# Performance work log

Measured on AMD Instinct MI355X. Metric: run time of the kernel, lower is better.

## Reference

```python
import jax, jax.numpy as jnp
import numpy as np

L, H, NH, F = 6, 1024, 16, 4096
B, S = 4, 512
D = H // NH
LN_EPS = 1e-12
GELU_C = 0.7978845608028654  # sqrt(2/pi)


def gelu_new(x):
    return 0.5 * x * (1.0 + jnp.tanh(GELU_C * (x + 0.044715 * x * x * x)))


def layer_norm(x, ln):
    # ln: [2, H] -> gamma, beta
    m = jnp.mean(x, axis=-1, keepdims=True)
    v = jnp.mean(jnp.square(x - m), axis=-1, keepdims=True)
    return (x - m) * jax.lax.rsqrt(v + LN_EPS) * ln[0] + ln[1]


def attention(q_in, kv_in, mask, qkv_w, qkv_b):
    # qkv_w: [3, H, H], qkv_b: [3, H]; mask: [B, S_kv] (1 = keep)
    b, s_q, _ = q_in.shape
    s_kv = kv_in.shape[1]
    q = (q_in @ qkv_w[0] + qkv_b[0]).reshape(b, s_q, NH, D)
    k = (kv_in @ qkv_w[1] + qkv_b[1]).reshape(b, s_kv, NH, D)
    v = (kv_in @ qkv_w[2] + qkv_b[2]).reshape(b, s_kv, NH, D)
    scale = 1.0 / (D ** 0.5)
    score = jnp.einsum('bind,bjnd->bnij', q, k) * scale  # [B, NH, Sq, Skv]
    adder = (1.0 - mask.astype(score.dtype))[:, None, None, :] * -10000.0
    prob = jax.nn.softmax(score + adder, axis=-1)
    out = jnp.einsum('bnij,bjnd->bind', prob, v)
    return out.reshape(b, s_q, H)


def _forward(hidden_states, encoder_hidden_states, attention_mask, encoder_attention_mask,
             sa_qkv_w, sa_qkv_b, sa_out_w, sa_out_b, sa_ln,
             ca_qkv_w, ca_qkv_b, ca_out_w, ca_out_b, ca_ln,
             o1_w, o1_b, o1_ln, ffn_w, ffn_b, o2_w, o2_b, o2_ln):
    h = hidden_states
    for i in range(L):
        # self attention + dense/dropout/LN (residual = h)
        self_vec = attention(h, h, attention_mask, sa_qkv_w[i], sa_qkv_b[i])
        attn_out = layer_norm(self_vec @ sa_out_w[i] + sa_out_b[i] + h, sa_ln[i])
        # cross attention + dense/dropout/LN (residual = h, per original code)
        cross_vec = attention(h, encoder_hidden_states, encoder_attention_mask,
                              ca_qkv_w[i], ca_qkv_b[i])
        cross_out = layer_norm(cross_vec @ ca_out_w[i] + ca_out_b[i] + h, ca_ln[i])
        # output_1: dense(attn_out) + cross_out, then LN
        attn_out = layer_norm(attn_out @ o1_w[i] + o1_b[i] + cross_out, o1_ln[i])
        # FFN with gelu_new, output_2: dense(inter) + attn_out, then LN
        inter = gelu_new(attn_out @ ffn_w[i] + ffn_b[i])
        h = layer_norm(inter @ o2_w[i] + o2_b[i] + attn_out, o2_ln[i])
    return h


def setup_inputs() -> dict:
    key = jax.random.key(0)
    ks = jax.random.split(key, 16)
    std = 0.02
    w = lambda k, shape: (jax.random.normal(k, shape, jnp.float32) * std)
    ln_init = jnp.stack([jnp.ones((L, H), jnp.float32), jnp.zeros((L, H), jnp.float32)], axis=1)
    return {
        'hidden_states': jax.random.normal(ks[0], (B, S, H), jnp.float32),
        'encoder_hidden_states': jax.random.normal(ks[1], (B, S, H), jnp.float32),
        'attention_mask': jnp.ones((B, S), jnp.int32),
        'encoder_attention_mask': jnp.ones((B, S), jnp.int32),
        'sa_qkv_w': w(ks[2], (L, 3, H, H)), 'sa_qkv_b': w(ks[3], (L, 3, H)),
        'sa_out_w': w(ks[4], (L, H, H)), 'sa_out_b': w(ks[5], (L, H)), 'sa_ln': ln_init,
        'ca_qkv_w': w(ks[6], (L, 3, H, H)), 'ca_qkv_b': w(ks[7], (L, 3, H)),
        'ca_out_w': w(ks[8], (L, H, H)), 'ca_out_b': w(ks[9], (L, H)), 'ca_ln': ln_init,
        'o1_w': w(ks[10], (L, H, H)), 'o1_b': w(ks[11], (L, H)), 'o1_ln': ln_init,
        'ffn_w': w(ks[12], (L, H, F)), 'ffn_b': w(ks[13], (L, F)),
        'o2_w': w(ks[14], (L, F, H)), 'o2_b': w(ks[15], (L, H)), 'o2_ln': ln_init,
    }


def reference(hidden_states, encoder_hidden_states, attention_mask, encoder_attention_mask,
              sa_qkv_w, sa_qkv_b, sa_out_w, sa_out_b, sa_ln,
              ca_qkv_w, ca_qkv_b, ca_out_w, ca_out_b, ca_ln,
              o1_w, o1_b, o1_ln, ffn_w, ffn_b, o2_w, o2_b, o2_ln):
    return _forward(hidden_states, encoder_hidden_states, attention_mask, encoder_attention_mask,
                    sa_qkv_w, sa_qkv_b, sa_out_w, sa_out_b, sa_ln,
                    ca_qkv_w, ca_qkv_b, ca_out_w, ca_out_b, ca_ln,
                    o1_w, o1_b, o1_ln, ffn_w, ffn_b, o2_w, o2_b, o2_ln)
```

## Files before the change

kernel.cpp:

```cpp
#include <hip/hip_runtime.h>


#define LNUM 6
#define HDIM 1024
#define NHEAD 16
#define DHEAD 64
#define BDIM 4
#define SDIM 512
#define FDIM 4096
#define MROWS (BDIM * SDIM)
#define HSQ (HDIM * HDIM)

typedef __bf16 bf16_t;
typedef bf16_t bf16x8 __attribute__((ext_vector_type(8)));
typedef float f32x4 __attribute__((ext_vector_type(4)));

__device__ __forceinline__ float bf2f(unsigned short u) {
    union { unsigned int i; float f; } x;
    x.i = ((unsigned int)u) << 16;
    return x.f;
}

__device__ __forceinline__ unsigned short f2bf(float f) {
    union { float f; unsigned int i; } u;
    u.f = f;
    unsigned int x = u.i;
    unsigned int lsb = (x >> 16) & 1u;
    x += 0x7fffu + lsb;
    return (unsigned short)(x >> 16);
}

__device__ __forceinline__ void async16(const unsigned short* g, unsigned short* l) {
    __builtin_amdgcn_global_load_lds(
        (const __attribute__((address_space(1))) unsigned int*)g,
        (__attribute__((address_space(3))) unsigned int*)l, 16, 0, 0);
}

template<int N>
__device__ __forceinline__ void s_wait_vmcnt() {
    asm volatile("s_waitcnt vmcnt(%0)" :: "n"(N) : "memory");
}

template<int BM, int BN, bool GELU, bool OUTBF16>
__global__ __launch_bounds__(256) void mfma_gemm(
    const unsigned short* __restrict__ A,
    const unsigned short* __restrict__ BT,
    const float* __restrict__ bias,
    void* __restrict__ Cv,
    int M, int N, int K)
{
    constexpr int BK = 64;
    constexpr int MI = BM / 32;
    constexpr int NJ = BN / 32;
    constexpr int LPT = BM / 32 + BN / 32;

    __shared__ unsigned short As[2][BM][BK];
    __shared__ unsigned short Bs[2][BN][BK];

    const int t = threadIdx.x;
    const int w = t >> 6;
    const int lane = t & 63;
    const int quad = lane >> 4;
    const int cm = lane & 15;
    const int wrow = (w >> 1) * (BM / 2);
    const int wcol = (w & 1) * (BN / 2);
    const int row0 = blockIdx.x * BM;
    const int col0 = blockIdx.y * BN;

    f32x4 acc[MI][NJ] = {};

    const int lrow = lane >> 3;
    const int lcol = ((lane & 7) ^ lrow) * 8;
    const int sw = cm & 7;

    auto stage = [&](int buf, int k0) {
#pragma unroll
        for (int j = 0; j < BM / 32; ++j) {
            int mb = w * (BM / 4) + j * 8;
            async16(A + (size_t)(row0 + mb + lrow) * K + k0 + lcol, &As[buf][mb][0]);
        }
#pragma unroll
        for (int j = 0; j < BN / 32; ++j) {
            int nb = w * (BN / 4) + j * 8;
            async16(BT + (size_t)(col0 + nb + lrow) * K + k0 + lcol, &Bs[buf][nb][0]);
        }
    };

    const int NT = K / BK;
    stage(0, 0);
    int cur = 0;
    for (int ti = 0; ti < NT; ++ti) {
        if (ti + 1 < NT) {
            stage(cur ^ 1, (ti + 1) * BK);
            s_wait_vmcnt<LPT>();
        } else {
            s_wait_vmcnt<0>();
        }
        __builtin_amdgcn_s_barrier();
        __builtin_amdgcn_sched_barrier(0);

#pragma unroll
        for (int kk = 0; kk < BK; kk += 32) {
            const int cc = kk >> 3;
            bf16x8 av[MI], bv[NJ];
#pragma unroll
            for (int i = 0; i < MI; ++i)
                av[i] = *(const bf16x8*)&As[cur][wrow + 16 * i + cm][((cc + quad) ^ sw) * 8];
#pragma unroll
            for (int j = 0; j < NJ; ++j)
                bv[j] = *(const bf16x8*)&Bs[cur][wcol + 16 * j + cm][((cc + quad) ^ sw) * 8];
#pragma unroll
            for (int i = 0; i < MI; ++i)
#pragma unroll
                for (int j = 0; j < NJ; ++j)
                    acc[i][j] = __builtin_amdgcn_mfma_f32_16x16x32_bf16(
                        av[i], bv[j], acc[i][j], 0, 0, 0);
        }

        __builtin_amdgcn_sched_barrier(0);
        __builtin_amdgcn_s_barrier();
        cur ^= 1;
    }

#pragma unroll
    for (int j = 0; j < NJ; ++j) {
        int col = col0 + wcol + 16 * j + cm;
        float bb = bias[col];
#pragma unroll
        for (int i = 0; i < MI; ++i) {
#pragma unroll
            for (int r = 0; r < 4; ++r) {
                int row = row0 + wrow + 16 * i + quad * 4 + r;
                float c = acc[i][j][r] + bb;
                if (GELU) {
                    float u = 0.7978845608028654f * (c + 0.044715f * c * c * c);
                    c = 0.5f * c * (1.0f + tanhf(u));
                }
                if (OUTBF16)
                    ((unsigned short*)Cv)[(size_t)row * N + col] = f2bf(c);
                else
                    ((float*)Cv)[(size_t)row * N + col] = c;
            }
        }
    }
}

template<int BM>
__global__ __launch_bounds__(256) void mfma_gemm_qkv(
    const unsigned short* __restrict__ Aq,
    const unsigned short* __restrict__ Akv,
    const unsigned short* __restrict__ BT,
    const float* __restrict__ bias,
    unsigned short* __restrict__ qo,
    unsigned short* __restrict__ ko,
    unsigned short* __restrict__ vo,
    int M, int K)
{
    constexpr int BK = 64;
    constexpr int BN = 64;
    constexpr int MI = BM / 32;
    constexpr int NJ = 2;
    constexpr int LPT = BM / 32 + BN / 32;

    __shared__ unsigned short As[2][BM][BK];
    __shared__ unsigned short Bs[2][BN][BK];

    const int t = threadIdx.x;
    const int w = t >> 6;
    const int lane = t & 63;
    const int quad = lane >> 4;
    const int cm = lane & 15;
    const int wrow = (w >> 1) * (BM / 2);
    const int wcol = (w & 1) * 32;
    const int row0 = blockIdx.x * BM;
    const int col0 = blockIdx.y * BN;

    const int which = col0 >> 10;
    const unsigned short* __restrict__ A = (which == 0) ? Aq : Akv;

    f32x4 acc[MI][NJ] = {};

    const int lrow = lane >> 3;
    const int lcol = ((lane & 7) ^ lrow) * 8;
    const int sw = cm & 7;

    auto stage = [&](int buf, int k0) {
#pragma unroll
        for (int j = 0; j < BM / 32; ++j) {
            int mb = w * (BM / 4) + j * 8;
            async16(A + (size_t)(row0 + mb + lrow) * K + k0 + lcol, &As[buf][mb][0]);
        }
#pragma unroll
        for (int j = 0; j < NJ; ++j) {
            int nb = w * 16 + j * 8;
            async16(BT + (size_t)(col0 + nb + lrow) * K + k0 + lcol, &Bs[buf][nb][0]);
        }
    };

    const int NT = K / BK;
    stage(0, 0);
    int cur = 0;
    for (int ti = 0; ti < NT; ++ti) {
        if (ti + 1 < NT) {
            stage(cur ^ 1, (ti + 1) * BK);
            s_wait_vmcnt<LPT>();
        } else {
            s_wait_vmcnt<0>();
        }
        __builtin_amdgcn_s_barrier();
        __builtin_amdgcn_sched_barrier(0);

#pragma unroll
        for (int kk = 0; kk < BK; kk += 32) {
            const int cc = kk >> 3;
            bf16x8 av[MI], bv[NJ];
#pragma unroll
            for (int i = 0; i < MI; ++i)
                av[i] = *(const bf16x8*)&As[cur][wrow + 16 * i + cm][((cc + quad) ^ sw) * 8];
#pragma unroll
            for (int j = 0; j < NJ; ++j)
                bv[j] = *(const bf16x8*)&Bs[cur][wcol + 16 * j + cm][((cc + quad) ^ sw) * 8];
#pragma unroll
            for (int i = 0; i < MI; ++i)
#pragma unroll
                for (int j = 0; j < NJ; ++j)
                    acc[i][j] = __builtin_amdgcn_mfma_f32_16x16x32_bf16(
                        av[i], bv[j], acc[i][j], 0, 0, 0);
        }

        __builtin_amdgcn_sched_barrier(0);
        __builtin_amdgcn_s_barrier();
        cur ^= 1;
    }

    unsigned short* dst = (which == 0) ? qo : (which == 1) ? ko : vo;
    const int cbase = col0 & 1023;

#pragma unroll
    for (int j = 0; j < NJ; ++j) {
        int col = col0 + wcol + 16 * j + cm;
        float bb = bias[col];
        int coll = cbase + wcol + 16 * j + cm;
#pragma unroll
        for (int i = 0; i < MI; ++i) {
#pragma unroll
            for (int r = 0; r < 4; ++r) {
                int row = row0 + wrow + 16 * i + quad * 4 + r;
                dst[(size_t)row * HDIM + coll] = f2bf(acc[i][j][r] + bb);
            }
        }
    }
}

__global__ __launch_bounds__(256) void flash_attn(
    const unsigned short* __restrict__ q,
    const unsigned short* __restrict__ k,
    const unsigned short* __restrict__ v,
    const int* __restrict__ mask,
    unsigned short* __restrict__ ctx)
{
    __shared__ unsigned short Qs[64][64];
    __shared__ unsigned short Ks[64][64];
    __shared__ unsigned short Vs[64][72];
    __shared__ unsigned short Ps[4][16][72];

    const int t = threadIdx.x;
    const int w = t >> 6;
    const int lane = t & 63;
    const int quad = lane >> 4;
    const int cm = lane & 15;
    const int sw = cm & 7;

    const int q0 = blockIdx.x * 64;
    const int h = blockIdx.y;
    const int b = blockIdx.z;
    const size_t rowbase = (size_t)b * SDIM;
    const int hoff = h * DHEAD;

#pragma unroll
    for (int l = 0; l < 2; ++l) {
        int idx = t + l * 256;
        int r = idx >> 3;
        int c = idx & 7;
        *(uint4*)&Qs[r][((c ^ (r & 7)) * 8)] =
            *(const uint4*)(q + (rowbase + q0 + r) * HDIM + hoff + c * 8);
    }

    float m_prev[4] = {-1e30f, -1e30f, -1e30f, -1e30f};
    float l_sum[4] = {0.0f, 0.0f, 0.0f, 0.0f};
    f32x4 oacc[4] = {};

    for (int j0 = 0; j0 < SDIM; j0 += 64) {
        __syncthreads();
#pragma unroll
        for (int l = 0; l < 2; ++l) {
            int idx = t + l * 256;
            int r = idx >> 3;
            int c = idx & 7;
            *(uint4*)&Ks[r][((c ^ (r & 7)) * 8)] =
                *(const uint4*)(k + (rowbase + j0 + r) * HDIM + hoff + c * 8);
        }
#pragma unroll
        for (int l = 0; l < 4; ++l) {
            int idx = t + l * 256;
            int jj = idx >> 4;
            int d0 = (idx & 15) * 4;
            ushort4 vv = *(const ushort4*)(v + (rowbase + j0 + jj) * HDIM + hoff + d0);
            Vs[d0 + 0][jj] = vv.x;
            Vs[d0 + 1][jj] = vv.y;
            Vs[d0 + 2][jj] = vv.z;
            Vs[d0 + 3][jj] = vv.w;
        }
        __syncthreads();

        f32x4 sacc[4] = {};
#pragma unroll
        for (int kk = 0; kk < 64; kk += 32) {
            const int cc = kk >> 3;
            bf16x8 av = *(const bf16x8*)&Qs[w * 16 + cm][((cc + quad) ^ sw) * 8];
#pragma unroll
            for (int j2 = 0; j2 < 4; ++j2) {
                bf16x8 bv = *(const bf16x8*)&Ks[j2 * 16 + cm][((cc + quad) ^ sw) * 8];
                sacc[j2] = __builtin_amdgcn_mfma_f32_16x16x32_bf16(av, bv, sacc[j2], 0, 0, 0);
            }
        }

        float madd[4];
#pragma unroll
        for (int j2 = 0; j2 < 4; ++j2)
            madd[j2] = (1.0f - (float)mask[b * SDIM + j0 + j2 * 16 + cm]) * -10000.0f;

#pragma unroll
        for (int r = 0; r < 4; ++r) {
            float s0 = sacc[0][r] * 0.125f + madd[0];
            float s1 = sacc[1][r] * 0.125f + madd[1];
            float s2 = sacc[2][r] * 0.125f + madd[2];
            float s3 = sacc[3][r] * 0.125f + madd[3];
            float rm = fmaxf(fmaxf(s0, s1), fmaxf(s2, s3));
#pragma unroll
            for (int mo = 1; mo < 16; mo <<= 1)
                rm = fmaxf(rm, __shfl_xor(rm, mo, 64));
            float new_m = fmaxf(m_prev[r], rm);
            float alpha = __expf(m_prev[r] - new_m);
            m_prev[r] = new_m;
            float p0 = __expf(s0 - new_m);
            float p1 = __expf(s1 - new_m);
            float p2 = __expf(s2 - new_m);
            float p3 = __expf(s3 - new_m);
            float rs = p0 + p1 + p2 + p3;
#pragma unroll
            for (int mo = 1; mo < 16; mo <<= 1)
                rs += __shfl_xor(rs, mo, 64);
            l_sum[r] = l_sum[r] * alpha + rs;
#pragma unroll
            for (int d2 = 0; d2 < 4; ++d2)
                oacc[d2][r] *= alpha;
            int prow = quad * 4 + r;
            Ps[w][prow][0 * 16 + cm] = f2bf(p0);
            Ps[w][prow][1 * 16 + cm] = f2bf(p1);
            Ps[w][prow][2 * 16 + cm] = f2bf(p2);
            Ps[w][prow][3 * 16 + cm] = f2bf(p3);
        }

#pragma unroll
        for (int kk = 0; kk < 64; kk += 32) {
            bf16x8 pa = *(const bf16x8*)&Ps[w][cm][kk + quad * 8];
#pragma unroll
            for (int d2 = 0; d2 < 4; ++d2) {
                bf16x8 bv = *(const bf16x8*)&Vs[d2 * 16 + cm][kk + quad * 8];
                oacc[d2] = __builtin_amdgcn_mfma_f32_16x16x32_bf16(pa, bv, oacc[d2], 0, 0, 0);
            }
        }
    }

#pragma unroll
    for (int r = 0; r < 4; ++r) {
        float inv = 1.0f / l_sum[r];
        int row = q0 + w * 16 + quad * 4 + r;
#pragma unroll
        for (int d2 = 0; d2 < 4; ++d2) {
            ctx[(rowbase + row) * HDIM + hoff + d2 * 16 + cm] = f2bf(oacc[d2][r] * inv);
        }
    }
}

__global__ __launch_bounds__(256) void convtrans_all(
    const float* __restrict__ sqkv, const float* __restrict__ sout,
    const float* __restrict__ cqkv, const float* __restrict__ cout,
    const float* __restrict__ o1w,  const float* __restrict__ ffnw,
    const float* __restrict__ o2w,
    unsigned short* __restrict__ dq,  unsigned short* __restrict__ dso,
    unsigned short* __restrict__ dcq, unsigned short* __restrict__ dco,
    unsigned short* __restrict__ do1, unsigned short* __restrict__ dffn,
    unsigned short* __restrict__ do2)
{
    __shared__ unsigned short tile[64][72];
    const int bid = blockIdx.x;
    const float* src;
    unsigned short* dst;
    int K, N, tt;
    if (bid < 2304) {
        int m = bid >> 8;
        tt = bid & 255;
        K = HDIM; N = HDIM;
        if (m < 3)      { src = sqkv + (size_t)m * HSQ;       dst = dq  + (size_t)m * HSQ; }
        else if (m < 6) { src = cqkv + (size_t)(m - 3) * HSQ; dst = dcq + (size_t)(m - 3) * HSQ; }
        else if (m == 6){ src = sout; dst = dso; }
        else if (m == 7){ src = cout; dst = dco; }
        else            { src = o1w;  dst = do1; }
    } else if (bid < 3328) {
        tt = bid - 2304; K = HDIM; N = FDIM; src = ffnw; dst = dffn;
    } else {
        tt = bid - 3328; K = FDIM; N = HDIM; src = o2w; dst = do2;
    }
    const int tn = N >> 6;
    const int n0 = (tt % tn) * 64;
    const int k0 = (tt / tn) * 64;
    const int t = threadIdx.x;
#pragma unroll
    for (int l = 0; l < 4; ++l) {
        int idx = t + l * 256;
        int kk = idx >> 4;
        int nn = (idx & 15) * 4;
        float4 v = *(const float4*)(src + (size_t)(k0 + kk) * N + n0 + nn);
        tile[nn + 0][kk] = f2bf(v.x);
        tile[nn + 1][kk] = f2bf(v.y);
        tile[nn + 2][kk] = f2bf(v.z);
        tile[nn + 3][kk] = f2bf(v.w);
    }
    __syncthreads();
#pragma unroll
    for (int l = 0; l < 2; ++l) {
        int c = t + l * 256;
        int nn = c >> 3;
        int kk = (c & 7) * 8;
        *(uint4*)(dst + (size_t)(n0 + nn) * K + k0 + kk) = *(const uint4*)&tile[nn][kk];
    }
}

template<bool OUTF32>
__global__ __launch_bounds__(256) void ln_kernel(
    const float* __restrict__ x, const unsigned short* __restrict__ resid,
    const float* __restrict__ ln, void* __restrict__ out)
{
    const int row = blockIdx.x;
    const float* xr = x + (size_t)row * HDIM;
    const unsigned short* rr = resid + (size_t)row * HDIM;
    const int t = threadIdx.x;
    __shared__ float red[4];

    float4 xv = ((const float4*)xr)[t];
    ushort4 rv = ((const ushort4*)rr)[t];
    float z[4];
    z[0] = xv.x + bf2f(rv.x);
    z[1] = xv.y + bf2f(rv.y);
    z[2] = xv.z + bf2f(rv.z);
    z[3] = xv.w + bf2f(rv.w);
    float s = z[0] + z[1] + z[2] + z[3];
#pragma unroll
    for (int off = 32; off > 0; off >>= 1) s += __shfl_down(s, off, 64);
    if ((t & 63) == 0) red[t >> 6] = s;
    __syncthreads();
    s = red[0] + red[1] + red[2] + red[3];
    float mean = s * (1.0f / (float)HDIM);

    float vs = 0.0f;
#pragma unroll
    for (int i = 0; i < 4; ++i) {
        float d = z[i] - mean;
        vs += d * d;
    }
#pragma unroll
    for (int off = 32; off > 0; off >>= 1) vs += __shfl_down(vs, off, 64);
    __syncthreads();
    if ((t & 63) == 0) red[t >> 6] = vs;
    __syncthreads();
    vs = red[0] + red[1] + red[2] + red[3];
    float inv = rsqrtf(vs * (1.0f / (float)HDIM) + 1e-12f);

    const float* g = ln + 4 * t;
    const float* bb = ln + HDIM + 4 * t;
    if (OUTF32) {
        float4 o;
        o.x = (z[0] - mean) * inv * g[0] + bb[0];
        o.y = (z[1] - mean) * inv * g[1] + bb[1];
        o.z = (z[2] - mean) * inv * g[2] + bb[2];
        o.w = (z[3] - mean) * inv * g[3] + bb[3];
        ((float4*)((float*)out + (size_t)row * HDIM))[t] = o;
    } else {
        ushort4 o;
        o.x = f2bf((z[0] - mean) * inv * g[0] + bb[0]);
        o.y = f2bf((z[1] - mean) * inv * g[1] + bb[1]);
        o.z = f2bf((z[2] - mean) * inv * g[2] + bb[2]);
        o.w = f2bf((z[3] - mean) * inv * g[3] + bb[3]);
        ((ushort4*)((unsigned short*)out + (size_t)row * HDIM))[t] = o;
    }
}

__global__ __launch_bounds__(256) void cvt_bf16_kernel(
    const float* __restrict__ in, unsigned short* __restrict__ out, int n4)
{
    int i = blockIdx.x * 256 + threadIdx.x;
    if (i < n4) {
        float4 v = ((const float4*)in)[i];
        ushort4 o;
        o.x = f2bf(v.x); o.y = f2bf(v.y); o.z = f2bf(v.z); o.w = f2bf(v.w);
        ((ushort4*)out)[i] = o;
    }
}

extern "C" void kernel_launch(void* const* d_in, const int* in_sizes, int n_in,
                              void* d_out, int out_size, void* d_ws, size_t ws_size,
                              hipStream_t stream)
{
    const float* in_hidden = (const float*)d_in[0];
    const float* enc_f     = (const float*)d_in[1];
    const int* attn_mask   = (const int*)d_in[2];
    const int* enc_attn_mask = (const int*)d_in[3];
    const float* sa_qkv_w  = (const float*)d_in[4];
    const float* sa_qkv_b  = (const float*)d_in[5];
    const float* sa_out_w  = (const float*)d_in[6];
    const float* sa_out_b  = (const float*)d_in[7];
    const float* sa_ln     = (const float*)d_in[8];
    const float* ca_qkv_w  = (const float*)d_in[9];
    const float* ca_qkv_b  = (const float*)d_in[10];
    const float* ca_out_w  = (const float*)d_in[11];
    const float* ca_out_b  = (const float*)d_in[12];
    const float* ca_ln     = (const float*)d_in[13];
    const float* o1_w      = (const float*)d_in[14];
    const float* o1_b      = (const float*)d_in[15];
    const float* o1_ln     = (const float*)d_in[16];
    const float* ffn_w     = (const float*)d_in[17];
    const float* ffn_b     = (const float*)d_in[18];
    const float* o2_w      = (const float*)d_in[19];
    const float* o2_b      = (const float*)d_in[20];
    const float* o2_ln     = (const float*)d_in[21];

    const size_t MH  = (size_t)MROWS * HDIM;
    const size_t Hsq = (size_t)HDIM * HDIM;
    const size_t HF  = (size_t)HDIM * FDIM;

    char* p = (char*)d_ws;
    unsigned short* wbf = (unsigned short*)p; p += (9 * Hsq + 2 * HF) * 2;
    float* t2     = (float*)p; p += MH * 4;
    unsigned short* qb     = (unsigned short*)p; p += MH * 2;
    unsigned short* kb     = (unsigned short*)p; p += MH * 2;
    unsigned short* vb     = (unsigned short*)p; p += MH * 2;
    unsigned short* ctx    = (unsigned short*)p; p += MH * 2;
    unsigned short* h      = (unsigned short*)p; p += MH * 2;
    unsigned short* enc_bf = (unsigned short*)p; p += MH * 2;
    unsigned short* attn1  = (unsigned short*)p; p += MH * 2;
    unsigned short* crossb = (unsigned short*)p; p += MH * 2;
    unsigned short* attn2  = (unsigned short*)p; p += MH * 2;
    unsigned short* tmp8b  = (unsigned short*)p; p += (size_t)MROWS * FDIM * 2;

    unsigned short* w_saqkv = wbf;
    unsigned short* w_saout = wbf + 3 * Hsq;
    unsigned short* w_caqkv = wbf + 4 * Hsq;
    unsigned short* w_caout = wbf + 7 * Hsq;
    unsigned short* w_o1    = wbf + 8 * Hsq;
    unsigned short* w_ffn   = wbf + 9 * Hsq;
    unsigned short* w_o2    = wbf + 9 * Hsq + HF;

    cvt_bf16_kernel<<<(MH / 4 + 255) / 256, 256, 0, stream>>>(in_hidden, h, MH / 4);
    cvt_bf16_kernel<<<(MH / 4 + 255) / 256, 256, 0, stream>>>(enc_f, enc_bf, MH / 4);

    for (int l = 0; l < LNUM; ++l) {
        convtrans_all<<<4352, 256, 0, stream>>>(
            sa_qkv_w + (size_t)l * 3 * Hsq, sa_out_w + (size_t)l * Hsq,
            ca_qkv_w + (size_t)l * 3 * Hsq, ca_out_w + (size_t)l * Hsq,
            o1_w + (size_t)l * Hsq, ffn_w + (size_t)l * HF, o2_w + (size_t)l * HF,
            w_saqkv, w_saout, w_caqkv, w_caout, w_o1, w_ffn, w_o2);

        mfma_gemm_qkv<64><<<dim3(MROWS / 64, 3072 / 64), 256, 0, stream>>>(
            h, h, w_saqkv, sa_qkv_b + (size_t)l * 3 * HDIM, qb, kb, vb, MROWS, HDIM);
        flash_attn<<<dim3(SDIM / 64, NHEAD, BDIM), 256, 0, stream>>>(
            qb, kb, vb, attn_mask, ctx);
        mfma_gemm<64, 64, false, false><<<dim3(MROWS / 64, HDIM / 64), 256, 0, stream>>>(
            ctx, w_saout, sa_out_b + (size_t)l * HDIM, t2, MROWS, HDIM, HDIM);
        ln_kernel<false><<<MROWS, 256, 0, stream>>>(t2, h, sa_ln + (size_t)l * 2 * HDIM, attn1);

        mfma_gemm_qkv<64><<<dim3(MROWS / 64, 3072 / 64), 256, 0, stream>>>(
            h, enc_bf, w_caqkv, ca_qkv_b + (size_t)l * 3 * HDIM, qb, kb, vb, MROWS, HDIM);
        flash_attn<<<dim3(SDIM / 64, NHEAD, BDIM), 256, 0, stream>>>(
            qb, kb, vb, enc_attn_mask, ctx);
        mfma_gemm<64, 64, false, false><<<dim3(MROWS / 64, HDIM / 64), 256, 0, stream>>>(
            ctx, w_caout, ca_out_b + (size_t)l * HDIM, t2, MROWS, HDIM, HDIM);
        ln_kernel<false><<<MROWS, 256, 0, stream>>>(t2, h, ca_ln + (size_t)l * 2 * HDIM, crossb);

        mfma_gemm<64, 64, false, false><<<dim3(MROWS / 64, HDIM / 64), 256, 0, stream>>>(
            attn1, w_o1, o1_b + (size_t)l * HDIM, t2, MROWS, HDIM, HDIM);
        ln_kernel<false><<<MROWS, 256, 0, stream>>>(t2, crossb, o1_ln + (size_t)l * 2 * HDIM, attn2);

        mfma_gemm<64, 128, true, true><<<dim3(MROWS / 64, FDIM / 128), 256, 0, stream>>>(
            attn2, w_ffn, ffn_b + (size_t)l * FDIM, tmp8b, MROWS, FDIM, HDIM);
        mfma_gemm<64, 64, false, false><<<dim3(MROWS / 64, HDIM / 64), 256, 0, stream>>>(
            tmp8b, w_o2, o2_b + (size_t)l * HDIM, t2, MROWS, HDIM, FDIM);
        if (l == LNUM - 1)
            ln_kernel<true><<<MROWS, 256, 0, stream>>>(
                t2, attn2, o2_ln + (size_t)l * 2 * HDIM, (float*)d_out);
        else
            ln_kernel<false><<<MROWS, 256, 0, stream>>>(
                t2, attn2, o2_ln + (size_t)l * 2 * HDIM, h);
    }
}
```

Before: 2.012 ms.

## Batch self and cross attention branches into shared launches; triple-buffer GEMM loads

```diff
diff --git a/kernel.cpp b/kernel.cpp
--- a/kernel.cpp
+++ b/kernel.cpp
@@ -52,10 +52,10 @@
     constexpr int BK = 64;
     constexpr int MI = BM / 32;
     constexpr int NJ = BN / 32;
-    constexpr int LPT = BM / 32 + BN / 32;
-
-    __shared__ unsigned short As[2][BM][BK];
-    __shared__ unsigned short Bs[2][BN][BK];
+    constexpr int LPT = MI + NJ;
+
+    __shared__ unsigned short As[3][BM][BK];
+    __shared__ unsigned short Bs[3][BN][BK];
 
     const int t = threadIdx.x;
     const int w = t >> 6;
@@ -71,7 +71,7 @@
 
     const int lrow = lane >> 3;
     const int lcol = ((lane & 7) ^ lrow) * 8;
-    const int sw = cm & 7;
+    const int sw = cm & 15 & 7;
 
     auto stage = [&](int buf, int k0) {
 #pragma unroll
@@ -88,10 +88,13 @@
 
     const int NT = K / BK;
     stage(0, 0);
-    int cur = 0;
+    stage(1, BK);
+    int c0 = 0, c1 = 1, c2 = 2;
     for (int ti = 0; ti < NT; ++ti) {
-        if (ti + 1 < NT) {
-            stage(cur ^ 1, (ti + 1) * BK);
+        if (ti + 2 < NT) {
+            stage(c2, (ti + 2) * BK);
+            s_wait_vmcnt<2 * LPT>();
+        } else if (ti + 1 < NT) {
             s_wait_vmcnt<LPT>();
         } else {
             s_wait_vmcnt<0>();
@@ -105,10 +108,10 @@
             bf16x8 av[MI], bv[NJ];
 #pragma unroll
             for (int i = 0; i < MI; ++i)
-                av[i] = *(const bf16x8*)&As[cur][wrow + 16 * i + cm][((cc + quad) ^ sw) * 8];
+                av[i] = *(const bf16x8*)&As[c0][wrow + 16 * i + cm][((cc + quad) ^ sw) * 8];
 #pragma unroll
             for (int j = 0; j < NJ; ++j)
-                bv[j] = *(const bf16x8*)&Bs[cur][wcol + 16 * j + cm][((cc + quad) ^ sw) * 8];
+                bv[j] = *(const bf16x8*)&Bs[c0][wcol + 16 * j + cm][((cc + quad) ^ sw) * 8];
 #pragma unroll
             for (int i = 0; i < MI; ++i)
 #pragma unroll
@@ -119,7 +122,7 @@
 
         __builtin_amdgcn_sched_barrier(0);
         __builtin_amdgcn_s_barrier();
-        cur ^= 1;
+        int tmp = c0; c0 = c1; c1 = c2; c2 = tmp;
     }
 
 #pragma unroll
@@ -145,38 +148,39 @@
     }
 }
 
-template<int BM>
-__global__ __launch_bounds__(256) void mfma_gemm_qkv(
-    const unsigned short* __restrict__ Aq,
-    const unsigned short* __restrict__ Akv,
-    const unsigned short* __restrict__ BT,
-    const float* __restrict__ bias,
-    unsigned short* __restrict__ qo,
-    unsigned short* __restrict__ ko,
-    unsigned short* __restrict__ vo,
+__global__ __launch_bounds__(256) void mfma_gemm_qkv6(
+    const unsigned short* __restrict__ hA,
+    const unsigned short* __restrict__ encA,
+    const unsigned short* __restrict__ swq,
+    const unsigned short* __restrict__ cwq,
+    const float* __restrict__ sb, const float* __restrict__ cb,
+    unsigned short* __restrict__ q1, unsigned short* __restrict__ k1,
+    unsigned short* __restrict__ v1,
+    unsigned short* __restrict__ q2, unsigned short* __restrict__ k2,
+    unsigned short* __restrict__ v2,
     int M, int K)
 {
-    constexpr int BK = 64;
-    constexpr int BN = 64;
-    constexpr int MI = BM / 32;
-    constexpr int NJ = 2;
-    constexpr int LPT = BM / 32 + BN / 32;
-
-    __shared__ unsigned short As[2][BM][BK];
-    __shared__ unsigned short Bs[2][BN][BK];
+    constexpr int BM = 64, BN = 64, BK = 64;
+    constexpr int MI = 2, NJ = 2, LPT = 4;
+
+    __shared__ unsigned short As[3][BM][BK];
+    __shared__ unsigned short Bs[3][BN][BK];
 
     const int t = threadIdx.x;
     const int w = t >> 6;
     const int lane = t & 63;
     const int quad = lane >> 4;
     const int cm = lane & 15;
-    const int wrow = (w >> 1) * (BM / 2);
+    const int wrow = (w >> 1) * 32;
     const int wcol = (w & 1) * 32;
     const int row0 = blockIdx.x * BM;
     const int col0 = blockIdx.y * BN;
 
-    const int which = col0 >> 10;
-    const unsigned short* __restrict__ A = (which == 0) ? Aq : Akv;
+    const int sec = col0 >> 10;
+    const unsigned short* __restrict__ A = (sec <= 3) ? hA : encA;
+    const unsigned short* __restrict__ BT =
+        (sec < 3) ? swq + (size_t)col0 * K : cwq + (size_t)(col0 - 3072) * K;
+    const float* __restrict__ bias = (sec < 3) ? sb + col0 : cb + (col0 - 3072);
 
     f32x4 acc[MI][NJ] = {};
 
@@ -186,23 +190,26 @@
 
     auto stage = [&](int buf, int k0) {
 #pragma unroll
-        for (int j = 0; j < BM / 32; ++j) {
-            int mb = w * (BM / 4) + j * 8;
+        for (int j = 0; j < 2; ++j) {
+            int mb = w * 16 + j * 8;
             async16(A + (size_t)(row0 + mb + lrow) * K + k0 + lcol, &As[buf][mb][0]);
         }
 #pragma unroll
-        for (int j = 0; j < NJ; ++j) {
+        for (int j = 0; j < 2; ++j) {
             int nb = w * 16 + j * 8;
-            async16(BT + (size_t)(col0 + nb + lrow) * K + k0 + lcol, &Bs[buf][nb][0]);
+            async16(BT + (size_t)(nb + lrow) * K + k0 + lcol, &Bs[buf][nb][0]);
         }
     };
 
     const int NT = K / BK;
     stage(0, 0);
-    int cur = 0;
+    stage(1, BK);
+    int c0 = 0, c1 = 1, c2 = 2;
     for (int ti = 0; ti < NT; ++ti) {
-        if (ti + 1 < NT) {
-            stage(cur ^ 1, (ti + 1) * BK);
+        if (ti + 2 < NT) {
+            stage(c2, (ti + 2) * BK);
+            s_wait_vmcnt<2 * LPT>();
+        } else if (ti + 1 < NT) {
             s_wait_vmcnt<LPT>();
         } else {
             s_wait_vmcnt<0>();
@@ -211,15 +218,15 @@
         __builtin_amdgcn_sched_barrier(0);
 
 #pragma unroll
-        for (int kk = 0; kk < BK; kk += 32) {
+        for (int kk = 0; kk < 64; kk += 32) {
             const int cc = kk >> 3;
             bf16x8 av[MI], bv[NJ];
 #pragma unroll
             for (int i = 0; i < MI; ++i)
-                av[i] = *(const bf16x8*)&As[cur][wrow + 16 * i + cm][((cc + quad) ^ sw) * 8];
+                av[i] = *(const bf16x8*)&As[c0][wrow + 16 * i + cm][((cc + quad) ^ sw) * 8];
 #pragma unroll
             for (int j = 0; j < NJ; ++j)
-                bv[j] = *(const bf16x8*)&Bs[cur][wcol + 16 * j + cm][((cc + quad) ^ sw) * 8];
+                bv[j] = *(const bf16x8*)&Bs[c0][wcol + 16 * j + cm][((cc + quad) ^ sw) * 8];
 #pragma unroll
             for (int i = 0; i < MI; ++i)
 #pragma unroll
@@ -230,16 +237,16 @@
 
         __builtin_amdgcn_sched_barrier(0);
         __builtin_amdgcn_s_barrier();
-        cur ^= 1;
-    }
-
-    unsigned short* dst = (which == 0) ? qo : (which == 1) ? ko : vo;
+        int tmp = c0; c0 = c1; c1 = c2; c2 = tmp;
+    }
+
+    unsigned short* dst = sec == 0 ? q1 : sec == 1 ? k1 : sec == 2 ? v1
+                        : sec == 3 ? q2 : sec == 4 ? k2 : v2;
     const int cbase = col0 & 1023;
 
 #pragma unroll
     for (int j = 0; j < NJ; ++j) {
-        int col = col0 + wcol + 16 * j + cm;
-        float bb = bias[col];
+        float bb = bias[wcol + 16 * j + cm];
         int coll = cbase + wcol + 16 * j + cm;
 #pragma unroll
         for (int i = 0; i < MI; ++i) {
@@ -252,12 +259,115 @@
     }
 }
 
+__global__ __launch_bounds__(256) void mfma_gemm_out2(
+    const unsigned short* __restrict__ A0, const unsigned short* __restrict__ B0,
+    const float* __restrict__ b0, float* __restrict__ C0,
+    const unsigned short* __restrict__ A1, const unsigned short* __restrict__ B1,
+    const float* __restrict__ b1, float* __restrict__ C1,
+    int M, int N, int K)
+{
+    constexpr int BM = 64, BN = 64, BK = 64;
+    constexpr int MI = 2, NJ = 2, LPT = 4;
+
+    __shared__ unsigned short As[3][BM][BK];
+    __shared__ unsigned short Bs[3][BN][BK];
+
+    const int z = blockIdx.z;
+    const unsigned short* __restrict__ A  = z ? A1 : A0;
+    const unsigned short* __restrict__ BT = z ? B1 : B0;
+    const float* __restrict__ bias = z ? b1 : b0;
+    float* __restrict__ Cv = z ? C1 : C0;
+
+    const int t = threadIdx.x;
+    const int w = t >> 6;
+    const int lane = t & 63;
+    const int quad = lane >> 4;
+    const int cm = lane & 15;
+    const int wrow = (w >> 1) * 32;
+    const int wcol = (w & 1) * 32;
+    const int row0 = blockIdx.x * BM;
+    const int col0 = blockIdx.y * BN;
+
+    f32x4 acc[MI][NJ] = {};
+
+    const int lrow = lane >> 3;
+    const int lcol = ((lane & 7) ^ lrow) * 8;
+    const int sw = cm & 7;
+
+    auto stage = [&](int buf, int k0) {
+#pragma unroll
+        for (int j = 0; j < 2; ++j) {
+            int mb = w * 16 + j * 8;
+            async16(A + (size_t)(row0 + mb + lrow) * K + k0 + lcol, &As[buf][mb][0]);
+        }
+#pragma unroll
+        for (int j = 0; j < 2; ++j) {
+            int nb = w * 16 + j * 8;
+            async16(BT + (size_t)(col0 + nb + lrow) * K + k0 + lcol, &Bs[buf][nb][0]);
+        }
+    };
+
+    const int NT = K / BK;
+    stage(0, 0);
+    stage(1, BK);
+    int c0 = 0, c1 = 1, c2 = 2;
+    for (int ti = 0; ti < NT; ++ti) {
+        if (ti + 2 < NT) {
+            stage(c2, (ti + 2) * BK);
+            s_wait_vmcnt<2 * LPT>();
+        } else if (ti + 1 < NT) {
+            s_wait_vmcnt<LPT>();
+        } else {
+            s_wait_vmcnt<0>();
+        }
+        __builtin_amdgcn_s_barrier();
+        __builtin_amdgcn_sched_barrier(0);
+
+#pragma unroll
+        for (int kk = 0; kk < 64; kk += 32) {
+            const int cc = kk >> 3;
+            bf16x8 av[MI], bv[NJ];
+#pragma unroll
+            for (int i = 0; i < MI; ++i)
+                av[i] = *(const bf16x8*)&As[c0][wrow + 16 * i + cm][((cc + quad) ^ sw) * 8];
+#pragma unroll
+            for (int j = 0; j < NJ; ++j)
+                bv[j] = *(const bf16x8*)&Bs[c0][wcol + 16 * j + cm][((cc + quad) ^ sw) * 8];
+#pragma unroll
+            for (int i = 0; i < MI; ++i)
+#pragma unroll
+                for (int j = 0; j < NJ; ++j)
+                    acc[i][j] = __builtin_amdgcn_mfma_f32_16x16x32_bf16(
+                        av[i], bv[j], acc[i][j], 0, 0, 0);
+        }
+
+        __builtin_amdgcn_sched_barrier(0);
+        __builtin_amdgcn_s_barrier();
+        int tmp = c0; c0 = c1; c1 = c2; c2 = tmp;
+    }
+
+#pragma unroll
+    for (int j = 0; j < NJ; ++j) {
+        int col = col0 + wcol + 16 * j + cm;
+        float bb = bias[col];
+#pragma unroll
+        for (int i = 0; i < MI; ++i) {
+#pragma unroll
+            for (int r = 0; r < 4; ++r) {
+                int row = row0 + wrow + 16 * i + quad * 4 + r;
+                Cv[(size_t)row * N + col] = acc[i][j][r] + bb;
+            }
+        }
+    }
+}
+
 __global__ __launch_bounds__(256) void flash_attn(
-    const unsigned short* __restrict__ q,
-    const unsigned short* __restrict__ k,
-    const unsigned short* __restrict__ v,
-    const int* __restrict__ mask,
-    unsigned short* __restrict__ ctx)
+    const unsigned short* __restrict__ q1, const unsigned short* __restrict__ k1,
+    const unsigned short* __restrict__ v1,
+    const unsigned short* __restrict__ q2, const unsigned short* __restrict__ k2,
+    const unsigned short* __restrict__ v2,
+    const int* __restrict__ mask1, const int* __restrict__ mask2,
+    unsigned short* __restrict__ ctx1, unsigned short* __restrict__ ctx2)
 {
     __shared__ unsigned short Qs[64][64];
     __shared__ unsigned short Ks[64][64];
@@ -273,7 +383,15 @@
 
     const int q0 = blockIdx.x * 64;
     const int h = blockIdx.y;
-    const int b = blockIdx.z;
+    const int zz = blockIdx.z;
+    const int b = zz & (BDIM - 1);
+    const int which = zz >> 2;
+    const unsigned short* __restrict__ q = which ? q2 : q1;
+    const unsigned short* __restrict__ k = which ? k2 : k1;
+    const unsigned short* __restrict__ v = which ? v2 : v1;
+    const int* __restrict__ mask = which ? mask2 : mask1;
+    unsigned short* __restrict__ ctx = which ? ctx2 : ctx1;
+
     const size_t rowbase = (size_t)b * SDIM;
     const int hoff = h * DHEAD;
 
@@ -495,6 +613,62 @@
         o.w = f2bf((z[3] - mean) * inv * g[3] + bb[3]);
         ((ushort4*)((unsigned short*)out + (size_t)row * HDIM))[t] = o;
     }
+}
+
+__global__ __launch_bounds__(256) void ln2_kernel(
+    const float* __restrict__ xa, const float* __restrict__ xb,
+    const unsigned short* __restrict__ resid,
+    const float* __restrict__ lna, const float* __restrict__ lnb,
+    unsigned short* __restrict__ outa, unsigned short* __restrict__ outb)
+{
+    const int row = blockIdx.x;
+    const int z2 = blockIdx.y;
+    const float* x = z2 ? xb : xa;
+    const float* ln = z2 ? lnb : lna;
+    unsigned short* out = z2 ? outb : outa;
+
+    const float* xr = x + (size_t)row * HDIM;
+    const unsigned short* rr = resid + (size_t)row * HDIM;
+    const int t = threadIdx.x;
+    __shared__ float red[4];
+
+    float4 xv = ((const float4*)xr)[t];
+    ushort4 rv = ((const ushort4*)rr)[t];
+    float z[4];
+    z[0] = xv.x + bf2f(rv.x);
+    z[1] = xv.y + bf2f(rv.y);
+    z[2] = xv.z + bf2f(rv.z);
+    z[3] = xv.w + bf2f(rv.w);
+    float s = z[0] + z[1] + z[2] + z[3];
+#pragma unroll
+    for (int off = 32; off > 0; off >>= 1) s += __shfl_down(s, off, 64);
+    if ((t & 63) == 0) red[t >> 6] = s;
+    __syncthreads();
+    s = red[0] + red[1] + red[2] + red[3];
+    float mean = s * (1.0f / (float)HDIM);
+
+    float vs = 0.0f;
+#pragma unroll
+    for (int i = 0; i < 4; ++i) {
+        float d = z[i] - mean;
+        vs += d * d;
+    }
+#pragma unroll
+    for (int off = 32; off > 0; off >>= 1) vs += __shfl_down(vs, off, 64);
+    __syncthreads();
+    if ((t & 63) == 0) red[t >> 6] = vs;
+    __syncthreads();
+    vs = red[0] + red[1] + red[2] + red[3];
+    float inv = rsqrtf(vs * (1.0f / (float)HDIM) + 1e-12f);
+
+    const float* g = ln + 4 * t;
+    const float* bb = ln + HDIM + 4 * t;
+    ushort4 o;
+    o.x = f2bf((z[0] - mean) * inv * g[0] + bb[0]);
+    o.y = f2bf((z[1] - mean) * inv * g[1] + bb[1]);
+    o.z = f2bf((z[2] - mean) * inv * g[2] + bb[2]);
+    o.w = f2bf((z[3] - mean) * inv * g[3] + bb[3]);
+    ((ushort4*)(out + (size_t)row * HDIM))[t] = o;
 }
 
 __global__ __launch_bounds__(256) void cvt_bf16_kernel(
@@ -542,11 +716,16 @@
 
     char* p = (char*)d_ws;
     unsigned short* wbf = (unsigned short*)p; p += (9 * Hsq + 2 * HF) * 2;
-    float* t2     = (float*)p; p += MH * 4;
+    float* t2a    = (float*)p; p += MH * 4;
+    float* t2b    = (float*)p; p += MH * 4;
     unsigned short* qb     = (unsigned short*)p; p += MH * 2;
     unsigned short* kb     = (unsigned short*)p; p += MH * 2;
     unsigned short* vb     = (unsigned short*)p; p += MH * 2;
+    unsigned short* qb2    = (unsigned short*)p; p += MH * 2;
+    unsigned short* kb2    = (unsigned short*)p; p += MH * 2;
+    unsigned short* vb2    = (unsigned short*)p; p += MH * 2;
     unsigned short* ctx    = (unsigned short*)p; p += MH * 2;
+    unsigned short* ctx2   = (unsigned short*)p; p += MH * 2;
     unsigned short* h      = (unsigned short*)p; p += MH * 2;
     unsigned short* enc_bf = (unsigned short*)p; p += MH * 2;
     unsigned short* attn1  = (unsigned short*)p; p += MH * 2;
@@ -572,35 +751,36 @@
             o1_w + (size_t)l * Hsq, ffn_w + (size_t)l * HF, o2_w + (size_t)l * HF,
             w_saqkv, w_saout, w_caqkv, w_caout, w_o1, w_ffn, w_o2);
 
-        mfma_gemm_qkv<64><<<dim3(MROWS / 64, 3072 / 64), 256, 0, stream>>>(
-            h, h, w_saqkv, sa_qkv_b + (size_t)l * 3 * HDIM, qb, kb, vb, MROWS, HDIM);
-        flash_attn<<<dim3(SDIM / 64, NHEAD, BDIM), 256, 0, stream>>>(
-            qb, kb, vb, attn_mask, ctx);
+        mfma_gemm_qkv6<<<dim3(MROWS / 64, 6144 / 64), 256, 0, stream>>>(
+            h, enc_bf, w_saqkv, w_caqkv,
+            sa_qkv_b + (size_t)l * 3 * HDIM, ca_qkv_b + (size_t)l * 3 * HDIM,
+            qb, kb, vb, qb2, kb2, vb2, MROWS, HDIM);
+
+        flash_attn<<<dim3(SDIM / 64, NHEAD, 2 * BDIM), 256, 0, stream>>>(
+            qb, kb, vb, qb2, kb2, vb2, attn_mask, enc_attn_mask, ctx, ctx2);
+
+        mfma_gemm_out2<<<dim3(MROWS / 64, HDIM / 64, 2), 256, 0, stream>>>(
+            ctx, w_saout, sa_out_b + (size_t)l * HDIM, t2a,
+            ctx2, w_caout, ca_out_b + (size_t)l * HDIM, t2b,
+            MROWS, HDIM, HDIM);
+
+        ln2_kernel<<<dim3(MROWS, 2), 256, 0, stream>>>(
+            t2a, t2b, h, sa_ln + (size_t)l * 2 * HDIM, ca_ln + (size_t)l * 2 * HDIM,
+            attn1, crossb);
+
         mfma_gemm<64, 64, false, false><<<dim3(MROWS / 64, HDIM / 64), 256, 0, stream>>>(
-            ctx, w_saout, sa_out_b + (size_t)l * HDIM, t2, MROWS, HDIM, HDIM);
-        ln_kernel<false><<<MROWS, 256, 0, stream>>>(t2, h, sa_ln + (size_t)l * 2 * HDIM, attn1);
-
-        mfma_gemm_qkv<64><<<dim3(MROWS / 64, 3072 / 64), 256, 0, stream>>>(
-            h, enc_bf, w_caqkv, ca_qkv_b + (size_t)l * 3 * HDIM, qb, kb, vb, MROWS, HDIM);
-        flash_attn<<<dim3(SDIM / 64, NHEAD, BDIM), 256, 0, stream>>>(
-            qb, kb, vb, enc_attn_mask, ctx);
-        mfma_gemm<64, 64, false, false><<<dim3(MROWS / 64, HDIM / 64), 256, 0, stream>>>(
-            ctx, w_caout, ca_out_b + (size_t)l * HDIM, t2, MROWS, HDIM, HDIM);
-        ln_kernel<false><<<MROWS, 256, 0, stream>>>(t2, h, ca_ln + (size_t)l * 2 * HDIM, crossb);
-
-        mfma_gemm<64, 64, false, false><<<dim3(MROWS / 64, HDIM / 64), 256, 0, stream>>>(
-            attn1, w_o1, o1_b + (size_t)l * HDIM, t2, MROWS, HDIM, HDIM);
-        ln_kernel<false><<<MROWS, 256, 0, stream>>>(t2, crossb, o1_ln + (size_t)l * 2 * HDIM, attn2);
+            attn1, w_o1, o1_b + (size_t)l * HDIM, t2a, MROWS, HDIM, HDIM);
+        ln_kernel<false><<<MROWS, 256, 0, stream>>>(t2a, crossb, o1_ln + (size_t)l * 2 * HDIM, attn2);
 
         mfma_gemm<64, 128, true, true><<<dim3(MROWS / 64, FDIM / 128), 256, 0, stream>>>(
             attn2, w_ffn, ffn_b + (size_t)l * FDIM, tmp8b, MROWS, FDIM, HDIM);
         mfma_gemm<64, 64, false, false><<<dim3(MROWS / 64, HDIM / 64), 256, 0, stream>>>(
-            tmp8b, w_o2, o2_b + (size_t)l * HDIM, t2, MROWS, HDIM, FDIM);
+            tmp8b, w_o2, o2_b + (size_t)l * HDIM, t2a, MROWS, HDIM, FDIM);
         if (l == LNUM - 1)
             ln_kernel<true><<<MROWS, 256, 0, stream>>>(
-                t2, attn2, o2_ln + (size_t)l * 2 * HDIM, (float*)d_out);
+                t2a, attn2, o2_ln + (size_t)l * 2 * HDIM, (float*)d_out);
         else
             ln_kernel<false><<<MROWS, 256, 0, stream>>>(
-                t2, attn2, o2_ln + (size_t)l * 2 * HDIM, h);
-    }
-}
+                t2a, attn2, o2_ln + (size_t)l * 2 * HDIM, h);
+    }
+}
```

Result: faster. 1.786 ms (-11.2%).
